# Kernel tuning notes

Measured on AMD Instinct MI355X. Metric: run time of the kernel, lower is better.

The kernel has to match this reference:

```python
import jax, jax.numpy as jnp
import numpy as np

N = 100000
E = 1600000
F_IN = 128
HID = 64
HID2 = 32
NCLS = 2
EPS = 1e-5  # BatchNorm eps


def setup_inputs() -> dict:
    key = jax.random.key(0)
    ks = jax.random.split(key, 12)
    inp = {
        'x': jax.random.normal(ks[0], (N, F_IN), dtype=jnp.float32),
        'edge_index': jax.random.randint(ks[1], (2, E), 0, N, dtype=jnp.int64),
        # GCNConv layer 1: weight [F_IN, HID], bias [HID]
        'W1': jax.random.normal(ks[2], (F_IN, HID), dtype=jnp.float32) / np.sqrt(F_IN),
        'b1': jnp.zeros((HID,), dtype=jnp.float32),
        # GCNConv layer 2
        'W2': jax.random.normal(ks[3], (HID, HID2), dtype=jnp.float32) / np.sqrt(HID),
        'b2': jnp.zeros((HID2,), dtype=jnp.float32),
        # BatchNorm1d params (eval mode: running stats)
        'g1': jax.random.uniform(ks[4], (HID,), dtype=jnp.float32, minval=0.5, maxval=1.5),
        'be1': jax.random.normal(ks[5], (HID,), dtype=jnp.float32) * 0.1,
        'rm1': jax.random.normal(ks[6], (HID,), dtype=jnp.float32) * 0.1,
        'rv1': jax.random.uniform(ks[7], (HID,), dtype=jnp.float32, minval=0.5, maxval=1.5),
        'g2': jax.random.uniform(ks[8], (HID2,), dtype=jnp.float32, minval=0.5, maxval=1.5),
        'be2': jax.random.normal(ks[9], (HID2,), dtype=jnp.float32) * 0.1,
        'rm2': jax.random.normal(ks[10], (HID2,), dtype=jnp.float32) * 0.1,
        'rv2': jax.random.uniform(ks[11], (HID2,), dtype=jnp.float32, minval=0.5, maxval=1.5),
        # classifier
        'Wc': jax.random.normal(jax.random.fold_in(key, 99), (HID2, NCLS), dtype=jnp.float32) / np.sqrt(HID2),
        'bc': jnp.zeros((NCLS,), dtype=jnp.float32),
    }
    return inp


def _gcn_conv(x, src, dst, norm, W, b, n_nodes):
    # PyG GCNConv: transform -> gather source -> norm-weight -> scatter-add -> +bias
    h = x @ W                                  # [N, out]
    msg = h[src] * norm[:, None]               # [E+N, out] gathered messages
    out = jax.ops.segment_sum(msg, dst, num_segments=n_nodes)
    return out + b


def _bn_eval(x, gamma, beta, rmean, rvar):
    return (x - rmean) * (gamma * jax.lax.rsqrt(rvar + EPS)) + beta


def reference(x, edge_index, W1, b1, W2, b2, g1, be1, rm1, rv1, g2, be2, rm2, rv2, Wc, bc):
    n = x.shape[0]
    loop = jnp.arange(n, dtype=edge_index.dtype)
    src = jnp.concatenate([edge_index[0], loop])   # add self-loops
    dst = jnp.concatenate([edge_index[1], loop])
    # symmetric degree normalization on A + I (degree counted at target)
    deg = jax.ops.segment_sum(jnp.ones_like(dst, dtype=x.dtype), dst, num_segments=n)
    dinv = jnp.where(deg > 0, jax.lax.rsqrt(deg), 0.0)
    norm = dinv[src] * dinv[dst]                   # [E+N]

    h = _gcn_conv(x, src, dst, norm, W1, b1, n)
    h = jax.nn.relu(_bn_eval(h, g1, be1, rm1, rv1))
    # dropout: identity in eval mode
    h = _gcn_conv(h, src, dst, norm, W2, b2, n)
    h = jax.nn.relu(_bn_eval(h, g2, be2, rm2, rv2))
    logits = h @ Wc + bc
    return jax.nn.log_softmax(logits, axis=1)
```

## Files before the change

### kernel.cpp

```cpp
#include <hip/hip_runtime.h>
#include <hip/hip_fp16.h>
#include <math.h>

#define F_IN 128
#define HID 64
#define HID2 32
#define EPS_BN 1e-5f
#define BW 128
#define NBMAX 1024
#define CAP 2560
#define CH 8192

typedef _Float16 f16x8 __attribute__((ext_vector_type(8)));
typedef float f32x4 __attribute__((ext_vector_type(4)));

__global__ __launch_bounds__(1024) void partition_kernel(const int* __restrict__ src, const int* __restrict__ dst,
                                                         int E, int* __restrict__ gcursor,
                                                         unsigned* __restrict__ ebuf) {
    __shared__ int hist[NBMAX];
    __shared__ int start[NBMAX];
    __shared__ int cur[NBMAX];
    __shared__ int gb[NBMAX];
    __shared__ int sc[1024];
    __shared__ unsigned buf[CH];
    int tid = threadIdx.x;
    int e0 = blockIdx.x * CH;
    hist[tid] = 0;
    __syncthreads();
#pragma unroll
    for (int it = 0; it < CH / 1024; it++) {
        int e = e0 + tid + it * 1024;
        if (e < E) atomicAdd(&hist[dst[e] >> 7], 1);
    }
    __syncthreads();
    int v = hist[tid];
    sc[tid] = v;
    __syncthreads();
    for (int off = 1; off < 1024; off <<= 1) {
        int t = (tid >= off) ? sc[tid - off] : 0;
        __syncthreads();
        sc[tid] += t;
        __syncthreads();
    }
    int ex = sc[tid] - v;
    start[tid] = ex;
    cur[tid] = ex;
    gb[tid] = v ? atomicAdd(&gcursor[tid], v) : 0;
    __syncthreads();
#pragma unroll
    for (int it = 0; it < CH / 1024; it++) {
        int e = e0 + tid + it * 1024;
        if (e < E) {
            int d = dst[e], s = src[e];
            int p = atomicAdd(&cur[d >> 7], 1);
            buf[p] = ((unsigned)(d & (BW - 1)) << 17) | (unsigned)s;
        }
    }
    __syncthreads();
    int grp = tid >> 2, sub = tid & 3;
    for (int b = grp; b < NBMAX; b += 256) {
        int len = hist[b];
        if (!len) continue;
        int st = start[b];
        unsigned* dp = ebuf + (size_t)b * CAP + gb[b];
        for (int i = sub; i < len; i += 4) dp[i] = buf[st + i];
    }
}

__global__ __launch_bounds__(256) void localsort_kernel(unsigned* __restrict__ ebuf, const int* __restrict__ gcursor,
                                                        int* __restrict__ ns, int* __restrict__ ne,
                                                        float* __restrict__ dinv, int n) {
    __shared__ unsigned lbuf[CAP];
    __shared__ int lhist[BW];
    __shared__ int lcur[BW];
    __shared__ int stmp[256];
    int b = blockIdx.x;
    int tid = threadIdx.x;
    int base = b * CAP;
    int len = gcursor[b];
    int node0 = b * BW;
    int nn = min(BW, n - node0);
    if (tid < BW) lhist[tid] = 0;
    __syncthreads();
    for (int k = tid; k < len; k += 256) {
        unsigned u = ebuf[base + k];
        lbuf[k] = u;
        atomicAdd(&lhist[u >> 17], 1);
    }
    __syncthreads();
    int v = (tid < BW) ? lhist[tid] : 0;
    stmp[tid] = v;
    __syncthreads();
    for (int off = 1; off < 256; off <<= 1) {
        int t = (tid >= off) ? stmp[tid - off] : 0;
        __syncthreads();
        stmp[tid] += t;
        __syncthreads();
    }
    int ex = stmp[tid] - v;
    if (tid < BW) lcur[tid] = ex;
    if (tid < nn) {
        ns[node0 + tid] = base + ex;
        ne[node0 + tid] = base + ex + v;
        dinv[node0 + tid] = rsqrtf((float)(v + 1));
    }
    __syncthreads();
    for (int k = tid; k < len; k += 256) {
        unsigned u = lbuf[k];
        int p = atomicAdd(&lcur[u >> 17], 1);
        ebuf[base + p] = u & 0x1FFFFu;
    }
}

__global__ void constprep_kernel(const float* g1, const float* be1, const float* rm1, const float* rv1, const float* b1,
                                 const float* g2, const float* be2, const float* rm2, const float* rv2, const float* b2,
                                 float* A1, float* B1, float* A2, float* B2) {
    int t = threadIdx.x;
    if (t < HID)  { float s = g1[t] * rsqrtf(rv1[t] + EPS_BN); A1[t] = s; B1[t] = (b1[t] - rm1[t]) * s + be1[t]; }
    if (t < HID2) { float s = g2[t] * rsqrtf(rv2[t] + EPS_BN); A2[t] = s; B2[t] = (b2[t] - rm2[t]) * s + be2[t]; }
}

__global__ __launch_bounds__(256) void gemm1_kernel(const float* __restrict__ x, const float* __restrict__ W1,
                                                    const float* __restrict__ dinv, __half* __restrict__ ht1,
                                                    int n, int nwaves_tot) {
    __shared__ float wlds[F_IN * HID];
    int tid = threadIdx.x;
    {
        const float4* wv = (const float4*)W1;
        float4* wl = (float4*)wlds;
#pragma unroll
        for (int i = 0; i < F_IN * HID / 4 / 256; i++) wl[tid + 256 * i] = wv[tid + 256 * i];
    }
    __syncthreads();
    int lane = tid & 63;
    int l15 = lane & 15, lg = lane >> 4;
    f16x8 bf[4][4];
#pragma unroll
    for (int ks = 0; ks < 4; ks++) {
#pragma unroll
        for (int ct = 0; ct < 4; ct++) {
            int kb = ks * 32 + lg * 8;
            int col = ct * 16 + l15;
            f16x8 b;
#pragma unroll
            for (int e = 0; e < 8; e++) b[e] = (_Float16)wlds[(kb + e) * HID + col];
            bf[ks][ct] = b;
        }
    }
    int gw = blockIdx.x * 4 + (tid >> 6);
    int nrt = (n + 15) >> 4;
    for (int rt = gw; rt < nrt; rt += nwaves_tot) {
        int arow = rt * 16 + l15;
        const float* xr = x + (size_t)min(arow, n - 1) * F_IN;
        f32x4 acc[4];
#pragma unroll
        for (int ct = 0; ct < 4; ct++) acc[ct] = (f32x4){0.f, 0.f, 0.f, 0.f};
#pragma unroll
        for (int ks = 0; ks < 4; ks++) {
            float4 xa = *(const float4*)(xr + ks * 32 + lg * 8);
            float4 xb = *(const float4*)(xr + ks * 32 + lg * 8 + 4);
            f16x8 a;
            a[0] = (_Float16)xa.x; a[1] = (_Float16)xa.y; a[2] = (_Float16)xa.z; a[3] = (_Float16)xa.w;
            a[4] = (_Float16)xb.x; a[5] = (_Float16)xb.y; a[6] = (_Float16)xb.z; a[7] = (_Float16)xb.w;
#pragma unroll
            for (int ct = 0; ct < 4; ct++)
                acc[ct] = __builtin_amdgcn_mfma_f32_16x16x32_f16(a, bf[ks][ct], acc[ct], 0, 0, 0);
        }
        int rbase = rt * 16 + lg * 4;
#pragma unroll
        for (int reg = 0; reg < 4; reg++) {
            int row = rbase + reg;
            if (row < n) {
                float d = dinv[row];
                _Float16* dp = (_Float16*)ht1 + (size_t)row * HID + l15;
#pragma unroll
                for (int ct = 0; ct < 4; ct++)
                    dp[ct * 16] = (_Float16)(acc[ct][reg] * d);
            }
        }
    }
}

#define XP2 68
__global__ __launch_bounds__(256) void gemm2_kernel(const float* __restrict__ h1p, const float* __restrict__ W2,
                                                    const float* __restrict__ dinv, __half* __restrict__ ht2,
                                                    int n) {
    __shared__ float wlds[HID * HID2];
    __shared__ float xlds[64 * XP2];
    int tid = threadIdx.x;
    {
        const float4* wv = (const float4*)W2;
        float4* wl = (float4*)wlds;
#pragma unroll
        for (int i = 0; i < HID * HID2 / 4 / 256; i++) wl[tid + 256 * i] = wv[tid + 256 * i];
    }
    int row0 = blockIdx.x * 64;
    {
        const float4* xv = (const float4*)(h1p + (size_t)row0 * HID);
        int lim = (n - row0) * (HID / 4);
#pragma unroll
        for (int i = 0; i < 4; i++) {
            int f = tid + 256 * i;
            float4 v = make_float4(0.f, 0.f, 0.f, 0.f);
            if (f < lim) v = xv[f];
            int r = f >> 4, kp = (f & 15) * 4;
            *(float4*)&xlds[r * XP2 + kp] = v;
        }
    }
    __syncthreads();
    int col4 = (tid & 7) * 4;
    int rowg = tid >> 3;
    float acc[2][4];
#pragma unroll
    for (int r = 0; r < 2; r++)
#pragma unroll
        for (int c = 0; c < 4; c++) acc[r][c] = 0.f;
#pragma unroll 4
    for (int k = 0; k < HID; k += 4) {
        float4 wb[4];
#pragma unroll
        for (int j = 0; j < 4; j++) wb[j] = *(const float4*)&wlds[(k + j) * HID2 + col4];
#pragma unroll
        for (int r = 0; r < 2; r++) {
            float4 xa = *(const float4*)&xlds[(rowg * 2 + r) * XP2 + k];
            acc[r][0] = fmaf(xa.x, wb[0].x, acc[r][0]); acc[r][1] = fmaf(xa.x, wb[0].y, acc[r][1]);
            acc[r][2] = fmaf(xa.x, wb[0].z, acc[r][2]); acc[r][3] = fmaf(xa.x, wb[0].w, acc[r][3]);
            acc[r][0] = fmaf(xa.y, wb[1].x, acc[r][0]); acc[r][1] = fmaf(xa.y, wb[1].y, acc[r][1]);
            acc[r][2] = fmaf(xa.y, wb[1].z, acc[r][2]); acc[r][3] = fmaf(xa.y, wb[1].w, acc[r][3]);
            acc[r][0] = fmaf(xa.z, wb[2].x, acc[r][0]); acc[r][1] = fmaf(xa.z, wb[2].y, acc[r][1]);
            acc[r][2] = fmaf(xa.z, wb[2].z, acc[r][2]); acc[r][3] = fmaf(xa.z, wb[2].w, acc[r][3]);
            acc[r][0] = fmaf(xa.w, wb[3].x, acc[r][0]); acc[r][1] = fmaf(xa.w, wb[3].y, acc[r][1]);
            acc[r][2] = fmaf(xa.w, wb[3].z, acc[r][2]); acc[r][3] = fmaf(xa.w, wb[3].w, acc[r][3]);
        }
    }
    int rbase = row0 + rowg * 2;
#pragma unroll
    for (int r = 0; r < 2; r++) {
        int row = rbase + r;
        if (row < n) {
            float d = dinv[row];
            __half2 h0, h1;
            h0.x = __float2half(acc[r][0] * d); h0.y = __float2half(acc[r][1] * d);
            h1.x = __float2half(acc[r][2] * d); h1.y = __float2half(acc[r][3] * d);
            __half2* dp = (__half2*)(ht2 + (size_t)row * HID2 + col4);
            dp[0] = h0; dp[1] = h1;
        }
    }
}

__global__ __launch_bounds__(256) void agg1_kernel(const __half* __restrict__ ht1, const int* __restrict__ ns,
                                                   const int* __restrict__ ne, const int* __restrict__ csr,
                                                   const float* __restrict__ dinv,
                                                   const float* __restrict__ A1, const float* __restrict__ B1,
                                                   float* __restrict__ h1p, int n) {
    int node = (blockIdx.x * blockDim.x + threadIdx.x) >> 6;
    if (node >= n) return;
    int lane = threadIdx.x & 63;
    int eh = lane >> 5, cp = lane & 31;
    const __half2* htp = (const __half2*)ht1;
    int s = ns[node], e_end = ne[node];
    float ax = 0.f, ay = 0.f;
    if (eh == 0) {
        float2 f = __half22float2(htp[(size_t)node * 32 + cp]);
        ax = f.x; ay = f.y;
    }
    for (int i = s + eh; i < e_end; i += 16) {
        int idx[8];
        bool val[8];
#pragma unroll
        for (int j = 0; j < 8; j++) {
            int e = i + 2 * j;
            val[j] = e < e_end;
            idx[j] = csr[val[j] ? e : s];
        }
#pragma unroll
        for (int j = 0; j < 8; j++) {
            float2 f = __half22float2(htp[(size_t)idx[j] * 32 + cp]);
            ax += val[j] ? f.x : 0.f;
            ay += val[j] ? f.y : 0.f;
        }
    }
    ax += __shfl_xor(ax, 32);
    ay += __shfl_xor(ay, 32);
    if (eh == 0) {
        float d = dinv[node];
        int c0 = cp * 2;
        float2 o;
        o.x = fmaxf(fmaf(ax * d, A1[c0], B1[c0]), 0.f);
        o.y = fmaxf(fmaf(ay * d, A1[c0 + 1], B1[c0 + 1]), 0.f);
        *(float2*)&h1p[(size_t)node * HID + c0] = o;
    }
}

__global__ __launch_bounds__(256) void agg2_kernel(const __half* __restrict__ ht2, const int* __restrict__ ns,
                                                   const int* __restrict__ ne, const int* __restrict__ csr,
                                                   const float* __restrict__ dinv,
                                                   const float* __restrict__ A2, const float* __restrict__ B2,
                                                   const float* __restrict__ Wc, const float* __restrict__ bc,
                                                   float* __restrict__ out, int n) {
    int node = (blockIdx.x * blockDim.x + threadIdx.x) >> 6;
    if (node >= n) return;
    int lane = threadIdx.x & 63;
    int eq = lane >> 4, cp = lane & 15;
    const __half2* htp = (const __half2*)ht2;
    int s = ns[node], e_end = ne[node];
    float ax = 0.f, ay = 0.f;
    if (eq == 0) {
        float2 f = __half22float2(htp[(size_t)node * 16 + cp]);
        ax = f.x; ay = f.y;
    }
    for (int i = s + eq; i < e_end; i += 16) {
        int idx[4];
        bool val[4];
#pragma unroll
        for (int j = 0; j < 4; j++) {
            int e = i + 4 * j;
            val[j] = e < e_end;
            idx[j] = csr[val[j] ? e : s];
        }
#pragma unroll
        for (int j = 0; j < 4; j++) {
            float2 f = __half22float2(htp[(size_t)idx[j] * 16 + cp]);
            ax += val[j] ? f.x : 0.f;
            ay += val[j] ? f.y : 0.f;
        }
    }
    ax += __shfl_xor(ax, 32); ay += __shfl_xor(ay, 32);
    ax += __shfl_xor(ax, 16); ay += __shfl_xor(ay, 16);
    float d = dinv[node];
    int c0 = cp * 2;
    float v0 = fmaxf(fmaf(ax * d, A2[c0], B2[c0]), 0.f);
    float v1 = fmaxf(fmaf(ay * d, A2[c0 + 1], B2[c0 + 1]), 0.f);
    float p0 = v0 * Wc[c0 * 2 + 0] + v1 * Wc[c0 * 2 + 2];
    float p1 = v0 * Wc[c0 * 2 + 1] + v1 * Wc[c0 * 2 + 3];
#pragma unroll
    for (int off = 8; off >= 1; off >>= 1) { p0 += __shfl_xor(p0, off); p1 += __shfl_xor(p1, off); }
    if (lane == 0) {
        float l0 = p0 + bc[0], l1 = p1 + bc[1];
        float m = fmaxf(l0, l1);
        float lse = m + logf(expf(l0 - m) + expf(l1 - m));
        float2 o; o.x = l0 - lse; o.y = l1 - lse;
        *(float2*)&out[(size_t)node * 2] = o;
    }
}

extern "C" void kernel_launch(void* const* d_in, const int* in_sizes, int n_in,
                              void* d_out, int out_size, void* d_ws, size_t ws_size,
                              hipStream_t stream) {
    const float* x   = (const float*)d_in[0];
    const int*   ei  = (const int*)d_in[1];
    const float* W1  = (const float*)d_in[2];
    const float* b1  = (const float*)d_in[3];
    const float* W2  = (const float*)d_in[4];
    const float* b2  = (const float*)d_in[5];
    const float* g1  = (const float*)d_in[6];
    const float* be1 = (const float*)d_in[7];
    const float* rm1 = (const float*)d_in[8];
    const float* rv1 = (const float*)d_in[9];
    const float* g2  = (const float*)d_in[10];
    const float* be2 = (const float*)d_in[11];
    const float* rm2 = (const float*)d_in[12];
    const float* rv2 = (const float*)d_in[13];
    const float* Wc  = (const float*)d_in[14];
    const float* bc  = (const float*)d_in[15];
    float* out = (float*)d_out;

    int n = in_sizes[0] / F_IN;
    int E = in_sizes[1] / 2;
    const int* srcv = ei;
    const int* dstv = ei + E;
    int NB = (n + BW - 1) / BW;

    char* ws = (char*)d_ws;
    size_t off = 0;
    auto alloc = [&](size_t bytes) -> char* {
        char* r = ws + off;
        off = (off + bytes + 511) & ~(size_t)511;
        return r;
    };
    int*      gcursor = (int*)alloc((size_t)NB * 4);
    int*      ns      = (int*)alloc((size_t)n * 4);
    int*      ne      = (int*)alloc((size_t)n * 4);
    float*    dinv    = (float*)alloc((size_t)n * 4);
    float*    A1 = (float*)alloc(HID * 4);
    float*    B1 = (float*)alloc(HID * 4);
    float*    A2 = (float*)alloc(HID2 * 4);
    float*    B2 = (float*)alloc(HID2 * 4);
    unsigned* ebuf = (unsigned*)alloc((size_t)NB * CAP * 4);
    __half*   ht1  = (__half*)alloc((size_t)n * HID * 2);
    float*    h1p  = (float*)alloc((size_t)n * HID * 4);
    __half*   ht2  = ht1;

    hipMemsetAsync(gcursor, 0, (size_t)NB * 4, stream);

    int nch = (E + CH - 1) / CH;
    partition_kernel<<<nch, 1024, 0, stream>>>(srcv, dstv, E, gcursor, ebuf);
    localsort_kernel<<<NB, 256, 0, stream>>>(ebuf, gcursor, ns, ne, dinv, n);
    constprep_kernel<<<1, 64, 0, stream>>>(g1, be1, rm1, rv1, b1, g2, be2, rm2, rv2, b2, A1, B1, A2, B2);

    int g1blocks = 512;
    gemm1_kernel<<<g1blocks, 256, 0, stream>>>(x, W1, dinv, ht1, n, g1blocks * 4);
    agg1_kernel<<<(n + 3) / 4, 256, 0, stream>>>(ht1, ns, ne, (const int*)ebuf, dinv, A1, B1, h1p, n);
    int ngb = (n + 63) / 64;
    gemm2_kernel<<<ngb, 256, 0, stream>>>(h1p, W2, dinv, ht2, n);
    agg2_kernel<<<(n + 3) / 4, 256, 0, stream>>>(ht2, ns, ne, (const int*)ebuf, dinv, A2, B2, Wc, bc, out, n);
}
```

Measured before the change: 253.8 us.

## Remap aggregation lanes to per-feature columns with scalar wavefront edge indices

Both aggregation kernels are restructured. Edge ranges are now wave-uniform via readfirstlane, so CSR indices can be loaded as scalar/broadcast reads. Each lane owns one feature column and walks 16 edges per iteration, with a masked tail and tree-summed partial accumulators. This removes the cross-half shuffles and per-lane validity selects, and layer 2 uses two half-waves that split edges. The cost is fp16 scalar loads per lane instead of half2 vector loads, and some overread of csr past the end, which the padded ebuf allocation covers.

```diff
diff --git a/kernel.cpp b/kernel.cpp
--- a/kernel.cpp
+++ b/kernel.cpp
@@ -254,42 +254,42 @@
                                                    const float* __restrict__ A1, const float* __restrict__ B1,
                                                    float* __restrict__ h1p, int n) {
     int node = (blockIdx.x * blockDim.x + threadIdx.x) >> 6;
+    node = __builtin_amdgcn_readfirstlane(node);
     if (node >= n) return;
     int lane = threadIdx.x & 63;
-    int eh = lane >> 5, cp = lane & 31;
-    const __half2* htp = (const __half2*)ht1;
-    int s = ns[node], e_end = ne[node];
-    float ax = 0.f, ay = 0.f;
-    if (eh == 0) {
-        float2 f = __half22float2(htp[(size_t)node * 32 + cp]);
-        ax = f.x; ay = f.y;
-    }
-    for (int i = s + eh; i < e_end; i += 16) {
-        int idx[8];
-        bool val[8];
-#pragma unroll
-        for (int j = 0; j < 8; j++) {
-            int e = i + 2 * j;
-            val[j] = e < e_end;
-            idx[j] = csr[val[j] ? e : s];
-        }
-#pragma unroll
-        for (int j = 0; j < 8; j++) {
-            float2 f = __half22float2(htp[(size_t)idx[j] * 32 + cp]);
-            ax += val[j] ? f.x : 0.f;
-            ay += val[j] ? f.y : 0.f;
-        }
-    }
-    ax += __shfl_xor(ax, 32);
-    ay += __shfl_xor(ay, 32);
-    if (eh == 0) {
-        float d = dinv[node];
-        int c0 = cp * 2;
-        float2 o;
-        o.x = fmaxf(fmaf(ax * d, A1[c0], B1[c0]), 0.f);
-        o.y = fmaxf(fmaf(ay * d, A1[c0 + 1], B1[c0 + 1]), 0.f);
-        *(float2*)&h1p[(size_t)node * HID + c0] = o;
-    }
+    int s = __builtin_amdgcn_readfirstlane(ns[node]);
+    int e_end = __builtin_amdgcn_readfirstlane(ne[node]);
+    const _Float16* hp = (const _Float16*)ht1;
+    float acc = (float)hp[(size_t)node * HID + lane];
+    int i = s;
+    for (; i + 16 <= e_end; i += 16) {
+        int idx[16];
+#pragma unroll
+        for (int j = 0; j < 16; j++) idx[j] = csr[i + j];
+        float v[16];
+#pragma unroll
+        for (int j = 0; j < 16; j++) v[j] = (float)hp[(size_t)idx[j] * HID + lane];
+        float t0 = ((v[0] + v[1]) + (v[2] + v[3])) + ((v[4] + v[5]) + (v[6] + v[7]));
+        float t1 = ((v[8] + v[9]) + (v[10] + v[11])) + ((v[12] + v[13]) + (v[14] + v[15]));
+        acc += t0 + t1;
+    }
+    if (i < e_end) {
+        int idx[16];
+        float m[16];
+#pragma unroll
+        for (int j = 0; j < 16; j++) {
+            int e = i + j;
+            bool vb = e < e_end;
+            idx[j] = csr[vb ? e : s];
+            m[j] = vb ? 1.f : 0.f;
+        }
+#pragma unroll
+        for (int j = 0; j < 16; j++)
+            acc = fmaf((float)hp[(size_t)idx[j] * HID + lane], m[j], acc);
+    }
+    float d = dinv[node];
+    float o = fmaxf(fmaf(acc * d, A1[lane], B1[lane]), 0.f);
+    h1p[(size_t)node * HID + lane] = o;
 }
 
 __global__ __launch_bounds__(256) void agg2_kernel(const __half* __restrict__ ht2, const int* __restrict__ ns,
@@ -299,42 +299,48 @@
                                                    const float* __restrict__ Wc, const float* __restrict__ bc,
                                                    float* __restrict__ out, int n) {
     int node = (blockIdx.x * blockDim.x + threadIdx.x) >> 6;
+    node = __builtin_amdgcn_readfirstlane(node);
     if (node >= n) return;
     int lane = threadIdx.x & 63;
-    int eq = lane >> 4, cp = lane & 15;
-    const __half2* htp = (const __half2*)ht2;
-    int s = ns[node], e_end = ne[node];
-    float ax = 0.f, ay = 0.f;
-    if (eq == 0) {
-        float2 f = __half22float2(htp[(size_t)node * 16 + cp]);
-        ax = f.x; ay = f.y;
-    }
-    for (int i = s + eq; i < e_end; i += 16) {
-        int idx[4];
-        bool val[4];
-#pragma unroll
-        for (int j = 0; j < 4; j++) {
-            int e = i + 4 * j;
-            val[j] = e < e_end;
-            idx[j] = csr[val[j] ? e : s];
-        }
-#pragma unroll
-        for (int j = 0; j < 4; j++) {
-            float2 f = __half22float2(htp[(size_t)idx[j] * 16 + cp]);
-            ax += val[j] ? f.x : 0.f;
-            ay += val[j] ? f.y : 0.f;
-        }
-    }
-    ax += __shfl_xor(ax, 32); ay += __shfl_xor(ay, 32);
-    ax += __shfl_xor(ax, 16); ay += __shfl_xor(ay, 16);
+    int p = lane >> 5;
+    int c = lane & 31;
+    int s = __builtin_amdgcn_readfirstlane(ns[node]);
+    int e_end = __builtin_amdgcn_readfirstlane(ne[node]);
+    const _Float16* hp = (const _Float16*)ht2;
+    float acc = (p == 0) ? (float)hp[(size_t)node * HID2 + c] : 0.f;
+    int i = s;
+    for (; i + 16 <= e_end; i += 16) {
+        int idx[8];
+#pragma unroll
+        for (int j = 0; j < 8; j++) {
+            int ia = csr[i + 2 * j];
+            int ib = csr[i + 2 * j + 1];
+            idx[j] = p ? ib : ia;
+        }
+        float v[8];
+#pragma unroll
+        for (int j = 0; j < 8; j++) v[j] = (float)hp[(size_t)idx[j] * HID2 + c];
+        acc += ((v[0] + v[1]) + (v[2] + v[3])) + ((v[4] + v[5]) + (v[6] + v[7]));
+    }
+    if (i < e_end) {
+#pragma unroll
+        for (int j = 0; j < 8; j++) {
+            int ea = i + 2 * j, eb = ea + 1;
+            int ia = csr[(ea < e_end) ? ea : s];
+            int ib = csr[(eb < e_end) ? eb : s];
+            int idx = p ? ib : ia;
+            int e = ea + p;
+            float f = (float)hp[(size_t)idx * HID2 + c];
+            acc += (e < e_end) ? f : 0.f;
+        }
+    }
+    acc += __shfl_xor(acc, 32);
     float d = dinv[node];
-    int c0 = cp * 2;
-    float v0 = fmaxf(fmaf(ax * d, A2[c0], B2[c0]), 0.f);
-    float v1 = fmaxf(fmaf(ay * d, A2[c0 + 1], B2[c0 + 1]), 0.f);
-    float p0 = v0 * Wc[c0 * 2 + 0] + v1 * Wc[c0 * 2 + 2];
-    float p1 = v0 * Wc[c0 * 2 + 1] + v1 * Wc[c0 * 2 + 3];
-#pragma unroll
-    for (int off = 8; off >= 1; off >>= 1) { p0 += __shfl_xor(p0, off); p1 += __shfl_xor(p1, off); }
+    float v0 = fmaxf(fmaf(acc * d, A2[c], B2[c]), 0.f);
+    float p0 = v0 * Wc[c * 2 + 0];
+    float p1 = v0 * Wc[c * 2 + 1];
+#pragma unroll
+    for (int off = 16; off >= 1; off >>= 1) { p0 += __shfl_xor(p0, off); p1 += __shfl_xor(p1, off); }
     if (lane == 0) {
         float l0 = p0 + bc[0], l1 = p1 + bc[1];
         float m = fmaxf(l0, l1);
@@ -386,7 +392,7 @@
     float*    B1 = (float*)alloc(HID * 4);
     float*    A2 = (float*)alloc(HID2 * 4);
     float*    B2 = (float*)alloc(HID2 * 4);
-    unsigned* ebuf = (unsigned*)alloc((size_t)NB * CAP * 4);
+    unsigned* ebuf = (unsigned*)alloc(((size_t)NB * CAP + 64) * 4);
     __half*   ht1  = (__half*)alloc((size_t)n * HID * 2);
     float*    h1p  = (float*)alloc((size_t)n * HID * 4);
     __half*   ht2  = ht1;
```

New measurement: 262.1 us. +3.3%, slower.
